# Kernel tuning notes

Hardware: AMD Instinct MI355X
Metric: run time of the kernel (lower is better)

The kernel has to match this reference:

```python
import jax, jax.numpy as jnp
import numpy as np

# ---- constants mirroring ATSSPostProcessor defaults / metainfo ----
PRE_NMS_THRESH = 0.05
PRE_NMS_TOP_N = 1000
NMS_THRESH = 0.6
POST_TOP_N = 100
IMG_H, IMG_W = 800.0, 1216.0      # metainfo img_shape
BW_XY, BW_WH = 10.0, 5.0          # GLIP/ATSS box coder weights (10,10,5,5)
MAX_DWH = float(np.log(1000.0 / 16.0))
CLASS_OFFSET = 10000.0            # batched_nms class offset (> max coord)


def setup_inputs() -> dict:
    key = jax.random.key(0)
    k0, k1, k2, k3 = jax.random.split(key, 4)
    N, C, L, H, W = 8, 80, 256, 100, 152
    box_regression = jax.random.normal(k0, (N, 4, H, W), jnp.float32)
    centerness = jax.random.normal(k1, (N, 1, H, W), jnp.float32)
    box_cls = jax.random.normal(k2, (N, C, H, W), jnp.float32)
    dot_product_logits = jax.random.normal(k3, (N, H * W, L), jnp.float32)
    # stride-8 grid anchors with base size 64
    ys, xs = np.meshgrid(np.arange(H), np.arange(W), indexing='ij')
    cx, cy = (xs + 0.5) * 8.0, (ys + 0.5) * 8.0
    anchors = jnp.asarray(
        np.stack([cx - 32, cy - 32, cx + 32, cy + 32], -1).reshape(-1, 4),
        jnp.float32)
    # MEAN aggregation positive map: class j <- tokens [3j, 3j+1, 3j+2]
    pm = np.zeros((C, L), np.float32)
    for j in range(C):
        pm[j, 3 * j:3 * j + 3] = 1.0 / 3.0
    pos_map = jnp.asarray(pm)
    return dict(box_regression=box_regression, centerness=centerness,
                box_cls=box_cls, dot_product_logits=dot_product_logits,
                anchors=anchors, pos_map=pos_map)


def _decode(a, r):
    # delta_xywh decode with weights (10,10,5,5), clamped to img_shape
    aw, ah = a[..., 2] - a[..., 0], a[..., 3] - a[..., 1]
    acx, acy = a[..., 0] + 0.5 * aw, a[..., 1] + 0.5 * ah
    dx, dy = r[..., 0] / BW_XY, r[..., 1] / BW_XY
    dw = jnp.minimum(r[..., 2] / BW_WH, MAX_DWH)
    dh = jnp.minimum(r[..., 3] / BW_WH, MAX_DWH)
    pcx, pcy = dx * aw + acx, dy * ah + acy
    pw, ph = jnp.exp(dw) * aw, jnp.exp(dh) * ah
    x1 = jnp.clip(pcx - 0.5 * pw, 0.0, IMG_W)
    y1 = jnp.clip(pcy - 0.5 * ph, 0.0, IMG_H)
    x2 = jnp.clip(pcx + 0.5 * pw, 0.0, IMG_W)
    y2 = jnp.clip(pcy + 0.5 * ph, 0.0, IMG_H)
    return jnp.stack([x1, y1, x2, y2], -1)


def _iou_matrix(b):  # b: [K,4]
    area = (b[:, 2] - b[:, 0]) * (b[:, 3] - b[:, 1])
    ix1 = jnp.maximum(b[:, None, 0], b[None, :, 0])
    iy1 = jnp.maximum(b[:, None, 1], b[None, :, 1])
    ix2 = jnp.minimum(b[:, None, 2], b[None, :, 2])
    iy2 = jnp.minimum(b[:, None, 3], b[None, :, 3])
    inter = jnp.maximum(ix2 - ix1, 0.0) * jnp.maximum(iy2 - iy1, 0.0)
    return inter / (area[:, None] + area[None, :] - inter + 1e-6)


def _nms_single(boxes, scores, labels, valid):
    # class-aware greedy NMS (batched_nms) on fixed-size K candidates
    K = boxes.shape[0]
    s = jnp.where(valid, scores, -1.0)
    order = jnp.argsort(-s)
    b, s, l, v = boxes[order], s[order], labels[order], valid[order]
    ob = b + (l.astype(b.dtype) * CLASS_OFFSET)[:, None]
    iou = _iou_matrix(ob)
    ar = jnp.arange(K)

    def body(i, keep):
        sup = keep[i] & (iou[i] > NMS_THRESH) & (ar > i)
        return keep & ~sup

    keep = jax.lax.fori_loop(0, K, body, v)
    s2 = jnp.where(keep, s, -1.0)
    topv, topi = jax.lax.top_k(s2, POST_TOP_N)
    good = topv > 0.0
    fb = jnp.where(good[:, None], b[topi], 0.0)
    fs = jnp.where(good, topv, 0.0)
    fl = jnp.where(good, l[topi], 0)
    return fb, fs, fl


def reference(box_regression, centerness, box_cls, dot_product_logits,
              anchors, pos_map):
    N = box_regression.shape[0]
    C = pos_map.shape[0]
    HW = anchors.shape[0]
    # permute_and_flatten: [N,4,H,W] -> [N,HW,4]
    reg = box_regression.transpose(0, 2, 3, 1).reshape(N, HW, 4)
    ctr = jax.nn.sigmoid(centerness.reshape(N, HW))
    # sigmoid score fusion + MEAN grounding->od aggregation
    dp = jax.nn.sigmoid(dot_product_logits)            # [N,HW,L]
    scores = jnp.einsum('nkl,cl->nkc', dp, pos_map)    # [N,HW,C]
    cand = scores > PRE_NMS_THRESH
    fused = scores * ctr[:, :, None]
    # dynamic per-image topk over candidates == fixed-K masked top_k
    masked = jnp.where(cand, fused, -1.0).reshape(N, HW * C)
    vals, idx = jax.lax.top_k(masked, PRE_NMS_TOP_N)   # [N,K]
    valid = jnp.take_along_axis(cand.reshape(N, -1), idx, axis=1)
    loc = idx // C
    labels = idx % C + 1
    a = anchors[loc]                                           # [N,K,4]
    r = jnp.take_along_axis(reg, loc[..., None], axis=1)       # [N,K,4]
    boxes = _decode(a, r)
    sc = jnp.sqrt(jnp.maximum(vals, 0.0))
    w = boxes[..., 2] - boxes[..., 0]
    h = boxes[..., 3] - boxes[..., 1]
    valid = valid & (w > 0) & (h > 0)  # min_size = 0 filter
    # scale_factor = 1.0 -> boxes unchanged
    out_boxes, out_scores, out_labels = jax.vmap(_nms_single)(
        boxes, sc, labels, valid)
    return out_boxes, out_scores, out_labels
```

## Files before the change

kernel.cpp:

```cpp
#include <hip/hip_runtime.h>
#include <hip/hip_bf16.h>

#define NIMG 8
#define NC   80
#define NL   256
#define HWQ  15200
#define TOPK 1000
#define CAP  4096
#define SSORT 2048
#define NPOST 100
#define PERIMG (HWQ * NC)
#define TOTAL (NIMG * PERIMG)
#define SROW 32
#define SBLK32 (NIMG * HWQ / SROW)
#define PI4  (PERIMG / 4)
#define WPI  (PI4 / 64)
#define NWAVE (NIMG * WPI)
#define CBLK (TOTAL / 4 / 256)

__device__ __forceinline__ unsigned flipKey(float f) {
    unsigned u = __float_as_uint(f);
    return u ^ (((unsigned)((int)u >> 31)) | 0x80000000u);
}
__device__ __forceinline__ float unflipKey(unsigned k) {
    unsigned u = k ^ ((k & 0x80000000u) ? 0x80000000u : 0xFFFFFFFFu);
    return __uint_as_float(u);
}
__device__ __forceinline__ float sigmoidf(float x) {
    return 1.0f / (1.0f + expf(-x));
}

__global__ void __launch_bounds__(256)
kinit(const float* __restrict__ pm, unsigned* nnz, unsigned* tok, float* wt,
      unsigned* __restrict__ gh) {
    int g = blockIdx.x * 256 + threadIdx.x;
    if (g < NIMG * 4096) gh[g] = 0;
    if (g < NC) {
        int c = g;
        int cnt = 0;
        for (int l = 0; l < NL; ++l) {
            float v = pm[c * NL + l];
            if (v != 0.0f) { tok[cnt * NC + c] = l; wt[cnt * NC + c] = v; cnt++; }
        }
        nnz[c] = cnt;
    }
}

__global__ void __launch_bounds__(512)
kscoreh(const float* __restrict__ dp, const float* __restrict__ cent,
        const unsigned* __restrict__ nnz, const unsigned* __restrict__ tok,
        const float* __restrict__ wt, float* __restrict__ scores,
        unsigned* __restrict__ gh) {
    __shared__ unsigned h[4096];
    __shared__ float sctr[SROW];
    int t = threadIdx.x;
    for (int i = t; i < 4096; i += 512) h[i] = 0;
    long long base = (long long)blockIdx.x * SROW;
    if (t < SROW) sctr[t] = sigmoidf(cent[base + t]);
    long long obase = base * NC;
    const float* dpb = dp + base * NL;

    int  rr[5], cc[5], mm[5];
    int  tk[5][3];
    float wv[5][3], xv[5][3];
#pragma unroll
    for (int j = 0; j < 5; ++j) {
        int o = t + j * 512;
        rr[j] = o / NC; cc[j] = o - rr[j] * NC;
        mm[j] = (int)nnz[cc[j]];
        int c = cc[j];
        tk[j][0] = (int)tok[c] & 255;
        tk[j][1] = (int)tok[NC + c] & 255;
        tk[j][2] = (int)tok[2 * NC + c] & 255;
        wv[j][0] = wt[c]; wv[j][1] = wt[NC + c]; wv[j][2] = wt[2 * NC + c];
    }
#pragma unroll
    for (int j = 0; j < 5; ++j) {
        const float* row = dpb + rr[j] * NL;
        if (tk[j][1] == tk[j][0] + 1 && tk[j][2] == tk[j][0] + 2) {
            float3 v3 = *(const float3*)(row + tk[j][0]);
            xv[j][0] = v3.x; xv[j][1] = v3.y; xv[j][2] = v3.z;
        } else {
            xv[j][0] = row[tk[j][0]];
            xv[j][1] = row[tk[j][1]];
            xv[j][2] = row[tk[j][2]];
        }
    }
    __syncthreads();
#pragma unroll
    for (int j = 0; j < 5; ++j) {
        float acc = 0.0f;
        if (mm[j] == 3) {
            float s0 = sigmoidf(xv[j][0]);
            float s1 = sigmoidf(xv[j][1]);
            float s2 = sigmoidf(xv[j][2]);
            acc += s0 * wv[j][0]; acc += s1 * wv[j][1]; acc += s2 * wv[j][2];
        } else {
            const float* row = dpb + rr[j] * NL;
            for (int q = 0; q < mm[j]; ++q)
                acc += sigmoidf(row[tok[q * NC + cc[j]]]) * wt[q * NC + cc[j]];
        }
        float sc = (acc > 0.05f) ? acc * sctr[rr[j]] : -1.0f;
        scores[obase + t + j * 512] = sc;
        atomicAdd(&h[flipKey(sc) >> 20], 1u);
    }
    __syncthreads();
    int n = (int)(base / HWQ);
    for (int i = t; i < 4096; i += 512)
        if (h[i]) atomicAdd(&gh[n * 4096 + i], h[i]);
}

__global__ void kfind1(const unsigned* __restrict__ gh, unsigned* meta) {
    __shared__ unsigned h[4096];
    __shared__ unsigned psum[256];
    int n = blockIdx.x;
    for (int i = threadIdx.x; i < 4096; i += 256) h[i] = gh[n * 4096 + i];
    __syncthreads();
    unsigned s = 0;
    for (int i = 0; i < 16; ++i) s += h[threadIdx.x * 16 + i];
    psum[threadIdx.x] = s;
    __syncthreads();
    if (threadIdx.x == 0) {
        unsigned cum = 0, above = 0; int B = 0; bool done = false;
        for (int seg = 255; seg >= 0 && !done; --seg) {
            if (cum + psum[seg] >= TOPK) {
                for (int b = seg * 16 + 15; b >= seg * 16; --b) {
                    if (cum + h[b] >= TOPK) { B = b; above = cum; done = true; break; }
                    cum += h[b];
                }
            } else cum += psum[seg];
        }
        meta[n] = (unsigned)B;
        meta[8 + n] = above;
    }
}

__global__ void __launch_bounds__(256)
kcountM(const float4* __restrict__ scores4, const unsigned* __restrict__ meta,
        unsigned* __restrict__ wavecnt, unsigned long long* __restrict__ wavemask) {
    int i4 = blockIdx.x * 256 + threadIdx.x;
    int n = i4 / PI4;
    unsigned B = meta[n];
    float4 v = scores4[i4];
    bool s0 = (flipKey(v.x) >> 20) >= B;
    bool s1 = (flipKey(v.y) >> 20) >= B;
    bool s2 = (flipKey(v.z) >> 20) >= B;
    bool s3 = (flipKey(v.w) >> 20) >= B;
    unsigned long long m0 = __ballot(s0);
    unsigned long long m1 = __ballot(s1);
    unsigned long long m2 = __ballot(s2);
    unsigned long long m3 = __ballot(s3);
    if ((threadIdx.x & 63) == 0) {
        int w = i4 >> 6;
        wavemask[(size_t)w * 4 + 0] = m0;
        wavemask[(size_t)w * 4 + 1] = m1;
        wavemask[(size_t)w * 4 + 2] = m2;
        wavemask[(size_t)w * 4 + 3] = m3;
        wavecnt[w] = (unsigned)(__popcll(m0) + __popcll(m1)
                              + __popcll(m2) + __popcll(m3));
    }
}

__global__ void __launch_bounds__(1024)
kscanW(const unsigned* __restrict__ wavecnt,
       const unsigned long long* __restrict__ wavemask,
       const float* __restrict__ scores,
       unsigned* __restrict__ cnt, unsigned long long* __restrict__ cand) {
    __shared__ unsigned ps[1024];
    int n = blockIdx.x, t = threadIdx.x;
    const unsigned* wc = wavecnt + n * WPI;
    int s0 = t * 5;
    unsigned loc[5], vv[5]; unsigned sum = 0;
#pragma unroll
    for (int j = 0; j < 5; ++j) {
        int i = s0 + j;
        unsigned x = (i < WPI) ? wc[i] : 0u;
        vv[j] = x; loc[j] = sum; sum += x;
    }
    ps[t] = sum;
    __syncthreads();
    for (int off = 1; off < 1024; off <<= 1) {
        unsigned add = (t >= off) ? ps[t - off] : 0u;
        __syncthreads();
        ps[t] += add;
        __syncthreads();
    }
    unsigned excl = (t > 0) ? ps[t - 1] : 0u;
    if (t == 1023) cnt[n] = ps[1023];
    const float* sb = scores + (size_t)n * PERIMG;
    unsigned long long* cb = cand + (size_t)n * CAP;
#pragma unroll
    for (int j = 0; j < 5; ++j) {
        int wl = s0 + j;
        if (wl < WPI && vv[j]) {
            unsigned off = excl + loc[j];
            const unsigned long long* mk = wavemask + ((size_t)(n * WPI + wl)) * 4;
#pragma unroll
            for (int e = 0; e < 4; ++e) {
                unsigned long long m = mk[e];
                while (m) {
                    int b = __ffsll(m) - 1; m &= m - 1;
                    int li = wl * 256 + b * 4 + e;
                    unsigned key = flipKey(sb[li]);
                    if (off < CAP)
                        cb[off] = ((unsigned long long)key << 32)
                                  | (unsigned)(~li);
                    off++;
                }
            }
        }
    }
}

__global__ void __launch_bounds__(256)
kcount(const float4* __restrict__ scores4, const unsigned* __restrict__ meta,
       unsigned* __restrict__ wavecnt) {
    int i4 = blockIdx.x * 256 + threadIdx.x;
    int n = i4 / PI4;
    unsigned B = meta[n];
    float4 v = scores4[i4];
    int ns = 0;
    ns += ((flipKey(v.x) >> 20) >= B);
    ns += ((flipKey(v.y) >> 20) >= B);
    ns += ((flipKey(v.z) >> 20) >= B);
    ns += ((flipKey(v.w) >> 20) >= B);
    int s = ns;
#pragma unroll
    for (int off = 1; off < 64; off <<= 1) s += __shfl_xor(s, off);
    if ((threadIdx.x & 63) == 0) wavecnt[i4 >> 6] = (unsigned)s;
}
__global__ void __launch_bounds__(1024)
kscan(const unsigned* __restrict__ wavecnt, unsigned* __restrict__ waveoff,
      unsigned* __restrict__ cnt) {
    __shared__ unsigned ps[1024];
    int n = blockIdx.x, t = threadIdx.x;
    const unsigned* wc = wavecnt + n * WPI;
    unsigned* wo = waveoff + n * WPI;
    int s0 = t * 5;
    unsigned loc[5]; unsigned sum = 0;
#pragma unroll
    for (int j = 0; j < 5; ++j) {
        int i = s0 + j;
        unsigned vv = (i < WPI) ? wc[i] : 0u;
        loc[j] = sum; sum += vv;
    }
    ps[t] = sum;
    __syncthreads();
    for (int off = 1; off < 1024; off <<= 1) {
        unsigned add = (t >= off) ? ps[t - off] : 0u;
        __syncthreads();
        ps[t] += add;
        __syncthreads();
    }
    unsigned excl = (t > 0) ? ps[t - 1] : 0u;
#pragma unroll
    for (int j = 0; j < 5; ++j) {
        int i = s0 + j;
        if (i < WPI) wo[i] = excl + loc[j];
    }
    if (t == 1023) cnt[n] = ps[1023];
}
__global__ void __launch_bounds__(256)
kwrite(const float4* __restrict__ scores4, const unsigned* __restrict__ meta,
       const unsigned* __restrict__ waveoff, unsigned long long* __restrict__ cand) {
    int i4 = blockIdx.x * 256 + threadIdx.x;
    int n = i4 / PI4;
    unsigned B = meta[n];
    float4 v = scores4[i4];
    int li0 = (i4 - n * PI4) * 4;
    unsigned keys[4]; int sel[4]; int ns = 0;
    keys[0] = flipKey(v.x); sel[0] = (keys[0] >> 20) >= B; ns += sel[0];
    keys[1] = flipKey(v.y); sel[1] = (keys[1] >> 20) >= B; ns += sel[1];
    keys[2] = flipKey(v.z); sel[2] = (keys[2] >> 20) >= B; ns += sel[2];
    keys[3] = flipKey(v.w); sel[3] = (keys[3] >> 20) >= B; ns += sel[3];
    int lane = threadIdx.x & 63;
    int pre = ns;
#pragma unroll
    for (int off = 1; off < 64; off <<= 1) {
        int o = __shfl_up(pre, off);
        if (lane >= off) pre += o;
    }
    unsigned base = waveoff[i4 >> 6] + (unsigned)(pre - ns);
    unsigned long long* cbase = cand + (size_t)n * CAP;
#pragma unroll
    for (int e = 0; e < 4; ++e) {
        if (sel[e]) {
            if (base < CAP)
                cbase[base] = ((unsigned long long)keys[e] << 32)
                              | (unsigned)(~(li0 + e));
            base++;
        }
    }
}

__global__ void __launch_bounds__(1024)
kfine(const unsigned long long* __restrict__ cand, const unsigned* __restrict__ cnt,
      const unsigned* __restrict__ meta, unsigned long long* __restrict__ sorted) {
    __shared__ unsigned h[4096];
    __shared__ unsigned long long sbuf[SSORT];
    __shared__ unsigned psum[256];
    __shared__ unsigned selcnt;
    __shared__ unsigned Fbin;
    int n = blockIdx.x, t = threadIdx.x;
    int M = min(cnt[n], (unsigned)CAP);
    unsigned B = meta[n], above = meta[8 + n];
    const unsigned long long* cb = cand + (size_t)n * CAP;
    for (int i = t; i < 4096; i += 1024) h[i] = 0;
    sbuf[t] = 0ULL; sbuf[t + 1024] = 0ULL;
    if (t == 0) selcnt = 0;
    __syncthreads();
    for (int i = t; i < M; i += 1024) {
        unsigned key = (unsigned)(cb[i] >> 32);
        if ((key >> 20) == B) atomicAdd(&h[(key >> 8) & 0xFFFu], 1u);
    }
    __syncthreads();
    if (t < 256) {
        unsigned s = 0;
        for (int i = 0; i < 16; ++i) s += h[t * 16 + i];
        psum[t] = s;
    }
    __syncthreads();
    if (t == 0) {
        unsigned cum = above; int F = 0; bool done = false;
        for (int seg = 255; seg >= 0 && !done; --seg) {
            if (cum + psum[seg] >= TOPK) {
                for (int b = seg * 16 + 15; b >= seg * 16; --b) {
                    if (cum + h[b] >= TOPK) { F = b; done = true; break; }
                    cum += h[b];
                }
            } else cum += psum[seg];
        }
        Fbin = (unsigned)F;
    }
    __syncthreads();
    unsigned T24 = (B << 12) | Fbin;
    for (int i = t; i < M; i += 1024) {
        unsigned long long e = cb[i];
        unsigned key = (unsigned)(e >> 32);
        if ((key >> 8) >= T24) {
            unsigned p = atomicAdd(&selcnt, 1u);
            if (p < SSORT) sbuf[p] = e;
        }
    }
    __syncthreads();
    int s = (int)selcnt;
    int SN = (s <= 1024) ? 1024 : SSORT;
    for (int k = 2; k <= SN; k <<= 1) {
        for (int j = k >> 1; j > 0; j >>= 1) {
            for (int i = t; i < SN; i += 1024) {
                int l = i ^ j;
                if (l > i) {
                    unsigned long long a = sbuf[i], b = sbuf[l];
                    bool sw = ((i & k) == 0) ? (a < b) : (a > b);
                    if (sw) { sbuf[i] = b; sbuf[l] = a; }
                }
            }
            __syncthreads();
        }
    }
    if (t < TOPK) sorted[(n << 10) + t] = sbuf[t];
}

__global__ void __launch_bounds__(256)
kdecode(const unsigned long long* __restrict__ sorted,
        const float* __restrict__ anchors, const float* __restrict__ breg,
        float4* __restrict__ box4, float4* __restrict__ obx4,
        float* __restrict__ areag, unsigned* __restrict__ lblkeep) {
    int gid = blockIdx.x * 256 + threadIdx.x;
    if (gid >= NIMG * TOPK) return;
    int n = gid / TOPK, r = gid - n * TOPK;
    int o = (n << 10) + r;
    unsigned long long e = sorted[o];
    unsigned key = (unsigned)(e >> 32);
    bool real = key > 0x80000000u;
    unsigned li = ~(unsigned)(e & 0xFFFFFFFFu);
    unsigned k = li / NC, c = li - k * NC;
    int label = (int)c + 1;
    float x1 = 0, y1 = 0, x2 = 0, y2 = 0;
    bool val = false;
    if (real) {
        float a0 = anchors[k * 4 + 0], a1 = anchors[k * 4 + 1];
        float a2 = anchors[k * 4 + 2], a3 = anchors[k * 4 + 3];
        float r0 = breg[(n * 4 + 0) * HWQ + k];
        float r1 = breg[(n * 4 + 1) * HWQ + k];
        float r2 = breg[(n * 4 + 2) * HWQ + k];
        float r3 = breg[(n * 4 + 3) * HWQ + k];
        float aw = a2 - a0, ah = a3 - a1;
        float acx = a0 + 0.5f * aw, acy = a1 + 0.5f * ah;
        float dx = r0 / 10.0f, dy = r1 / 10.0f;
        float dw = fminf(r2 / 5.0f, 4.135166556742356f);
        float dh = fminf(r3 / 5.0f, 4.135166556742356f);
        float pcx = dx * aw + acx, pcy = dy * ah + acy;
        float pw = expf(dw) * aw, ph = expf(dh) * ah;
        x1 = fminf(fmaxf(pcx - 0.5f * pw, 0.0f), 1216.0f);
        y1 = fminf(fmaxf(pcy - 0.5f * ph, 0.0f), 800.0f);
        x2 = fminf(fmaxf(pcx + 0.5f * pw, 0.0f), 1216.0f);
        y2 = fminf(fmaxf(pcy + 0.5f * ph, 0.0f), 800.0f);
        val = (x2 - x1 > 0.0f) && (y2 - y1 > 0.0f);
    }
    box4[o] = make_float4(x1, y1, x2, y2);
    float off = (float)label * 10000.0f;
    float o0 = x1 + off, o1 = y1 + off, o2 = x2 + off, o3 = y2 + off;
    obx4[o] = make_float4(o0, o1, o2, o3);
    areag[o] = (o2 - o0) * (o3 - o1);
    lblkeep[o] = (unsigned)(real ? label : 0) | ((val ? 1u : 0u) << 16);
}

__global__ void __launch_bounds__(1024)
knms2(const unsigned long long* __restrict__ sorted,
      const float4* __restrict__ obx4, const float* __restrict__ areag,
      const unsigned* __restrict__ lblkeep, const float4* __restrict__ box4,
      float* __restrict__ outBoxes, float* __restrict__ outScores,
      float* __restrict__ outLabels) {
    __shared__ float ob0[TOPK], ob1[TOPK], ob2[TOPK], ob3[TOPK], area[TOPK];
    __shared__ unsigned long long sup[TOPK];
    __shared__ unsigned short lbl[TOPK];
    __shared__ unsigned char  keepf[TOPK];
    __shared__ unsigned short wrank[TOPK];
    __shared__ unsigned short clist[TOPK];
    __shared__ unsigned short cstart[NC + 1];
    __shared__ unsigned ccnt[NC];
    __shared__ int pfx[1024];
    __shared__ int smax;

    int n = blockIdx.x, t = threadIdx.x;
    if (t < NC) ccnt[t] = 0;
    if (t == 0) smax = 0;
    if (t < TOPK) {
        int o = (n << 10) + t;
        float4 ob = obx4[o];
        ob0[t] = ob.x; ob1[t] = ob.y; ob2[t] = ob.z; ob3[t] = ob.w;
        area[t] = areag[o];
        unsigned lk = lblkeep[o];
        lbl[t] = (unsigned short)(lk & 0xFFFFu);
        keepf[t] = (unsigned char)(lk >> 16);
        sup[t] = 0ULL;
    }
    __syncthreads();

    if (t < TOPK) {
        unsigned short my = lbl[t];
        int w = 0;
        if (my) {
            for (int r = 0; r < t; ++r) w += (lbl[r] == my);
            atomicAdd(&ccnt[my - 1], 1u);
        }
        wrank[t] = (unsigned short)w;
    }
    __syncthreads();
    if (t < NC) atomicMax(&smax, (int)ccnt[t]);
    __syncthreads();
    if (t == 0) {
        unsigned s = 0;
        for (int c = 0; c < NC; ++c) { cstart[c] = (unsigned short)s; s += ccnt[c]; }
        cstart[NC] = (unsigned short)s;
    }
    __syncthreads();
    if (t < TOPK && lbl[t]) clist[cstart[lbl[t] - 1] + wrank[t]] = (unsigned short)t;
    __syncthreads();

    if (smax <= 64) {
        if (t < TOPK && lbl[t]) {
            int base = cstart[lbl[t] - 1];
            int w = wrank[t];
            float A0 = ob0[t], A1 = ob1[t], A2 = ob2[t], A3 = ob3[t], Aa = area[t];
            unsigned long long m = 0ULL;
            for (int j = 0; j < w; ++j) {
                int ib = clist[base + j];
                float iw = fminf(A2, ob2[ib]) - fmaxf(A0, ob0[ib]);
                float ih = fminf(A3, ob3[ib]) - fmaxf(A1, ob1[ib]);
                float inter = fmaxf(iw, 0.0f) * fmaxf(ih, 0.0f);
                float denom = Aa + area[ib] - inter + 1e-6f;
                if (inter / denom > 0.6f) m |= (1ull << j);
            }
            sup[t] = m;
        }
        __syncthreads();
        if (t < NC) {
            unsigned long long kb = 0ULL;
            int base = cstart[t], mc = (int)ccnt[t];
            for (int w = 0; w < mc; ++w) {
                int i = clist[base + w];
                bool kp = keepf[i] && ((sup[i] & kb) == 0ULL);
                keepf[i] = kp ? 1 : 0;
                if (kp) kb |= (1ull << w);
            }
        }
    } else {
        __syncthreads();
        if (t < NC) {
            int s0 = cstart[t], s1 = s0 + (int)ccnt[t];
            for (int a = s0; a < s1; ++a) {
                int ia = clist[a];
                if (!keepf[ia]) continue;
                float A0 = ob0[ia], A1 = ob1[ia], A2 = ob2[ia], A3 = ob3[ia];
                float Aa = area[ia];
                for (int b = a + 1; b < s1; ++b) {
                    int ib = clist[b];
                    if (!keepf[ib]) continue;
                    float iw = fminf(A2, ob2[ib]) - fmaxf(A0, ob0[ib]);
                    float ih = fminf(A3, ob3[ib]) - fmaxf(A1, ob1[ib]);
                    float inter = fmaxf(iw, 0.0f) * fmaxf(ih, 0.0f);
                    float denom = Aa + area[ib] - inter + 1e-6f;
                    if (inter / denom > 0.6f) keepf[ib] = 0;
                }
            }
        }
    }
    __syncthreads();

    pfx[t] = (t < TOPK) ? (int)keepf[t] : 0;
    __syncthreads();
    for (int off = 1; off < 1024; off <<= 1) {
        int add = (t >= off) ? pfx[t - off] : 0;
        __syncthreads();
        pfx[t] += add;
        __syncthreads();
    }
    int total = pfx[1023];

    if (t < TOPK && keepf[t]) {
        int q = pfx[t] - 1;
        if (q < NPOST) {
            int o = (n << 10) + t;
            float4 b = box4[o];
            float fused = unflipKey((unsigned)(sorted[o] >> 32));
            outBoxes[(n * NPOST + q) * 4 + 0] = b.x;
            outBoxes[(n * NPOST + q) * 4 + 1] = b.y;
            outBoxes[(n * NPOST + q) * 4 + 2] = b.z;
            outBoxes[(n * NPOST + q) * 4 + 3] = b.w;
            outScores[n * NPOST + q] = sqrtf(fmaxf(fused, 0.0f));
            outLabels[n * NPOST + q] = (float)lbl[t];
        }
    }
    if (t < NPOST && t >= total) {
        outBoxes[(n * NPOST + t) * 4 + 0] = 0.0f;
        outBoxes[(n * NPOST + t) * 4 + 1] = 0.0f;
        outBoxes[(n * NPOST + t) * 4 + 2] = 0.0f;
        outBoxes[(n * NPOST + t) * 4 + 3] = 0.0f;
        outScores[n * NPOST + t] = 0.0f;
        outLabels[n * NPOST + t] = 0.0f;
    }
}

extern "C" void kernel_launch(void* const* d_in, const int* in_sizes, int n_in,
                              void* d_out, int out_size, void* d_ws, size_t ws_size,
                              hipStream_t stream) {
    const float* breg = (const float*)d_in[0];
    const float* cent = (const float*)d_in[1];
    const float* dp   = (const float*)d_in[3];
    const float* anc  = (const float*)d_in[4];
    const float* pm   = (const float*)d_in[5];

    char* ws = (char*)d_ws;
    size_t off_scores  = 0;
    size_t off_gh      = off_scores + (size_t)TOTAL * 4;
    size_t off_cnt     = off_gh + (size_t)NIMG * 4096 * 4;
    size_t off_meta    = off_cnt + 128;
    size_t off_cand    = off_meta + 128;
    size_t off_nnz     = off_cand + (size_t)NIMG * CAP * 8;
    size_t off_tok     = off_nnz + 512;
    size_t off_wt      = off_tok + (size_t)NC * NL * 4;
    size_t off_wavecnt = off_wt + (size_t)NC * NL * 4;
    size_t off_tail    = off_wavecnt + (size_t)NWAVE * 4 + 64;
    size_t needed_new  = off_tail + (size_t)NWAVE * 32;
    size_t needed_old  = off_tail + (size_t)NWAVE * 4 + 64;
    if (ws_size < needed_old) return;
    bool useMask = ws_size >= needed_new;

    size_t off_sorted = off_scores;
    size_t off_box4   = off_sorted + (size_t)NIMG * 1024 * 8;
    size_t off_obx4   = off_box4 + (size_t)NIMG * 1024 * 16;
    size_t off_area   = off_obx4 + (size_t)NIMG * 1024 * 16;
    size_t off_lblk   = off_area + (size_t)NIMG * 1024 * 4;

    float*    scores  = (float*)(ws + off_scores);
    unsigned* gh      = (unsigned*)(ws + off_gh);
    unsigned* cnt     = (unsigned*)(ws + off_cnt);
    unsigned* meta    = (unsigned*)(ws + off_meta);
    unsigned long long* cand = (unsigned long long*)(ws + off_cand);
    unsigned* nnz     = (unsigned*)(ws + off_nnz);
    unsigned* tok     = (unsigned*)(ws + off_tok);
    float*    wt      = (float*)(ws + off_wt);
    unsigned* wavecnt = (unsigned*)(ws + off_wavecnt);
    unsigned long long* wavemask = (unsigned long long*)(ws + off_tail);
    unsigned* waveoff = (unsigned*)(ws + off_tail);
    unsigned long long* sorted = (unsigned long long*)(ws + off_sorted);
    float4*   box4    = (float4*)(ws + off_box4);
    float4*   obx4    = (float4*)(ws + off_obx4);
    float*    areag   = (float*)(ws + off_area);
    unsigned* lblkeep = (unsigned*)(ws + off_lblk);

    kinit<<<128, 256, 0, stream>>>(pm, nnz, tok, wt, gh);
    kscoreh<<<SBLK32, 512, 0, stream>>>(dp, cent, nnz, tok, wt, scores, gh);
    kfind1<<<NIMG, 256, 0, stream>>>(gh, meta);
    if (useMask) {
        kcountM<<<CBLK, 256, 0, stream>>>((const float4*)scores, meta,
                                          wavecnt, wavemask);
        kscanW<<<NIMG, 1024, 0, stream>>>(wavecnt, wavemask, scores, cnt, cand);
    } else {
        kcount<<<CBLK, 256, 0, stream>>>((const float4*)scores, meta, wavecnt);
        kscan<<<NIMG, 1024, 0, stream>>>(wavecnt, waveoff, cnt);
        kwrite<<<CBLK, 256, 0, stream>>>((const float4*)scores, meta, waveoff, cand);
    }
    kfine<<<NIMG, 1024, 0, stream>>>(cand, cnt, meta, sorted);
    kdecode<<<(NIMG * TOPK + 255) / 256, 256, 0, stream>>>(sorted, anc, breg,
                                                           box4, obx4, areag, lblkeep);

    float* outBoxes  = (float*)d_out;
    float* outScores = outBoxes + NIMG * NPOST * 4;
    float* outLabels = outScores + NIMG * NPOST;
    knms2<<<NIMG, 1024, 0, stream>>>(sorted, obx4, areag, lblkeep, box4,
                                     outBoxes, outScores, outLabels);
}
```

Baseline: 198.0 us.

## Stage sigmoid of full logit rows in LDS with coalesced float4 loads per wave

```diff
diff --git a/kernel.cpp b/kernel.cpp
--- a/kernel.cpp
+++ b/kernel.cpp
@@ -11,8 +11,8 @@
 #define NPOST 100
 #define PERIMG (HWQ * NC)
 #define TOTAL (NIMG * PERIMG)
-#define SROW 32
-#define SBLK32 (NIMG * HWQ / SROW)
+#define RPB  16
+#define SBLKR (NIMG * HWQ / RPB)
 #define PI4  (PERIMG / 4)
 #define WPI  (PI4 / 64)
 #define NWAVE (NIMG * WPI)
@@ -52,60 +52,55 @@
         const float* __restrict__ wt, float* __restrict__ scores,
         unsigned* __restrict__ gh) {
     __shared__ unsigned h[4096];
-    __shared__ float sctr[SROW];
+    __shared__ float sig[8][2][NL];
     int t = threadIdx.x;
+    int wid = t >> 6, lane = t & 63;
     for (int i = t; i < 4096; i += 512) h[i] = 0;
-    long long base = (long long)blockIdx.x * SROW;
-    if (t < SROW) sctr[t] = sigmoidf(cent[base + t]);
-    long long obase = base * NC;
-    const float* dpb = dp + base * NL;
-
-    int  rr[5], cc[5], mm[5];
-    int  tk[5][3];
-    float wv[5][3], xv[5][3];
-#pragma unroll
-    for (int j = 0; j < 5; ++j) {
-        int o = t + j * 512;
-        rr[j] = o / NC; cc[j] = o - rr[j] * NC;
-        mm[j] = (int)nnz[cc[j]];
-        int c = cc[j];
-        tk[j][0] = (int)tok[c] & 255;
-        tk[j][1] = (int)tok[NC + c] & 255;
-        tk[j][2] = (int)tok[2 * NC + c] & 255;
-        wv[j][0] = wt[c]; wv[j][1] = wt[NC + c]; wv[j][2] = wt[2 * NC + c];
-    }
-#pragma unroll
-    for (int j = 0; j < 5; ++j) {
-        const float* row = dpb + rr[j] * NL;
-        if (tk[j][1] == tk[j][0] + 1 && tk[j][2] == tk[j][0] + 2) {
-            float3 v3 = *(const float3*)(row + tk[j][0]);
-            xv[j][0] = v3.x; xv[j][1] = v3.y; xv[j][2] = v3.z;
-        } else {
-            xv[j][0] = row[tk[j][0]];
-            xv[j][1] = row[tk[j][1]];
-            xv[j][2] = row[tk[j][2]];
-        }
-    }
-    __syncthreads();
-#pragma unroll
-    for (int j = 0; j < 5; ++j) {
-        float acc = 0.0f;
-        if (mm[j] == 3) {
-            float s0 = sigmoidf(xv[j][0]);
-            float s1 = sigmoidf(xv[j][1]);
-            float s2 = sigmoidf(xv[j][2]);
-            acc += s0 * wv[j][0]; acc += s1 * wv[j][1]; acc += s2 * wv[j][2];
-        } else {
-            const float* row = dpb + rr[j] * NL;
-            for (int q = 0; q < mm[j]; ++q)
-                acc += sigmoidf(row[tok[q * NC + cc[j]]]) * wt[q * NC + cc[j]];
-        }
-        float sc = (acc > 0.05f) ? acc * sctr[rr[j]] : -1.0f;
-        scores[obase + t + j * 512] = sc;
-        atomicAdd(&h[flipKey(sc) >> 20], 1u);
-    }
-    __syncthreads();
-    int n = (int)(base / HWQ);
+    __syncthreads();
+    long long brow = (long long)blockIdx.x * RPB;
+    const float4* dp4 = (const float4*)dp;
+    float ctr2[2];
+#pragma unroll
+    for (int rr = 0; rr < 2; ++rr) {
+        long long row = brow + wid * 2 + rr;
+        float4 v = dp4[row * (NL / 4) + lane];
+        sig[wid][rr][lane * 4 + 0] = sigmoidf(v.x);
+        sig[wid][rr][lane * 4 + 1] = sigmoidf(v.y);
+        sig[wid][rr][lane * 4 + 2] = sigmoidf(v.z);
+        sig[wid][rr][lane * 4 + 3] = sigmoidf(v.w);
+        ctr2[rr] = sigmoidf(cent[row]);
+    }
+#pragma unroll
+    for (int p = 0; p < 2; ++p) {
+        int c = lane + p * 64;
+        if (c < NC) {
+            int m = (int)nnz[c];
+            int t0 = (int)tok[c] & 255;
+            int t1 = (int)tok[NC + c] & 255;
+            int t2 = (int)tok[2 * NC + c] & 255;
+            float w0 = wt[c], w1 = wt[NC + c], w2 = wt[2 * NC + c];
+#pragma unroll
+            for (int rr = 0; rr < 2; ++rr) {
+                long long row = brow + wid * 2 + rr;
+                const float* sg = sig[wid][rr];
+                float acc = 0.0f;
+                if (m == 3) {
+                    float s0 = sg[t0];
+                    float s1 = sg[t1];
+                    float s2 = sg[t2];
+                    acc += s0 * w0; acc += s1 * w1; acc += s2 * w2;
+                } else {
+                    for (int q = 0; q < m; ++q)
+                        acc += sg[(int)tok[q * NC + c] & 255] * wt[q * NC + c];
+                }
+                float sc = (acc > 0.05f) ? acc * ctr2[rr] : -1.0f;
+                scores[row * NC + c] = sc;
+                atomicAdd(&h[flipKey(sc) >> 20], 1u);
+            }
+        }
+    }
+    __syncthreads();
+    int n = (int)(brow / HWQ);
     for (int i = t; i < 4096; i += 512)
         if (h[i]) atomicAdd(&gh[n * 4096 + i], h[i]);
 }
@@ -592,7 +587,7 @@
     unsigned* lblkeep = (unsigned*)(ws + off_lblk);
 
     kinit<<<128, 256, 0, stream>>>(pm, nnz, tok, wt, gh);
-    kscoreh<<<SBLK32, 512, 0, stream>>>(dp, cent, nnz, tok, wt, scores, gh);
+    kscoreh<<<SBLKR, 512, 0, stream>>>(dp, cent, nnz, tok, wt, scores, gh);
     kfind1<<<NIMG, 256, 0, stream>>>(gh, meta);
     if (useMask) {
         kcountM<<<CBLK, 256, 0, stream>>>((const float4*)scores, meta,
```

New measurement: 212.7 us. 1.07x slower.

## Fuse candidate scan, fine select, sort, decode and NMS into one per-image kernel

Applied to the files above, without the earlier changes.

```diff
diff --git a/kernel.cpp b/kernel.cpp
--- a/kernel.cpp
+++ b/kernel.cpp
@@ -6,7 +6,6 @@
 #define NL   256
 #define HWQ  15200
 #define TOPK 1000
-#define CAP  4096
 #define SSORT 2048
 #define NPOST 100
 #define PERIMG (HWQ * NC)
@@ -162,158 +161,55 @@
 }
 
 __global__ void __launch_bounds__(1024)
-kscanW(const unsigned* __restrict__ wavecnt,
-       const unsigned long long* __restrict__ wavemask,
-       const float* __restrict__ scores,
-       unsigned* __restrict__ cnt, unsigned long long* __restrict__ cand) {
-    __shared__ unsigned ps[1024];
+ktail(const unsigned* __restrict__ wavecnt,
+      const unsigned long long* __restrict__ wavemask,
+      const float* __restrict__ scores, const unsigned* __restrict__ meta,
+      const float* __restrict__ anchors, const float* __restrict__ breg,
+      float* __restrict__ outBoxes, float* __restrict__ outScores,
+      float* __restrict__ outLabels) {
+    __shared__ unsigned long long sbuf[SSORT];
+    __shared__ unsigned uover[4096];
+    __shared__ float area[TOPK];
+    __shared__ unsigned long long sup[TOPK];
+    __shared__ unsigned short lbl[TOPK];
+    __shared__ unsigned char  keepf[TOPK];
+    __shared__ unsigned short wrank[TOPK];
+    __shared__ unsigned short clist[TOPK];
+    __shared__ unsigned short cstart[NC + 1];
+    __shared__ unsigned ccnt[NC];
+    __shared__ int pfx[1024];
+    __shared__ unsigned selcnt, FbinS;
+    __shared__ int smax;
+
     int n = blockIdx.x, t = threadIdx.x;
+    unsigned B = meta[n], above = meta[8 + n];
     const unsigned* wc = wavecnt + n * WPI;
-    int s0 = t * 5;
-    unsigned loc[5], vv[5]; unsigned sum = 0;
-#pragma unroll
-    for (int j = 0; j < 5; ++j) {
-        int i = s0 + j;
-        unsigned x = (i < WPI) ? wc[i] : 0u;
-        vv[j] = x; loc[j] = sum; sum += x;
-    }
-    ps[t] = sum;
-    __syncthreads();
-    for (int off = 1; off < 1024; off <<= 1) {
-        unsigned add = (t >= off) ? ps[t - off] : 0u;
-        __syncthreads();
-        ps[t] += add;
-        __syncthreads();
-    }
-    unsigned excl = (t > 0) ? ps[t - 1] : 0u;
-    if (t == 1023) cnt[n] = ps[1023];
+    const unsigned long long* wm = wavemask + (size_t)n * WPI * 4;
     const float* sb = scores + (size_t)n * PERIMG;
-    unsigned long long* cb = cand + (size_t)n * CAP;
-#pragma unroll
-    for (int j = 0; j < 5; ++j) {
-        int wl = s0 + j;
-        if (wl < WPI && vv[j]) {
-            unsigned off = excl + loc[j];
-            const unsigned long long* mk = wavemask + ((size_t)(n * WPI + wl)) * 4;
+
+    unsigned* h = uover;
+    for (int i = t; i < 4096; i += 1024) h[i] = 0;
+    sbuf[t] = 0ULL; sbuf[t + 1024] = 0ULL;
+    if (t == 0) { selcnt = 0; smax = 0; }
+    if (t < NC) ccnt[t] = 0;
+    __syncthreads();
+
+    for (int wl = t; wl < WPI; wl += 1024) {
+        if (wc[wl]) {
 #pragma unroll
             for (int e = 0; e < 4; ++e) {
-                unsigned long long m = mk[e];
+                unsigned long long m = wm[(size_t)wl * 4 + e];
                 while (m) {
                     int b = __ffsll(m) - 1; m &= m - 1;
-                    int li = wl * 256 + b * 4 + e;
-                    unsigned key = flipKey(sb[li]);
-                    if (off < CAP)
-                        cb[off] = ((unsigned long long)key << 32)
-                                  | (unsigned)(~li);
-                    off++;
-                }
-            }
-        }
-    }
-}
-
-__global__ void __launch_bounds__(256)
-kcount(const float4* __restrict__ scores4, const unsigned* __restrict__ meta,
-       unsigned* __restrict__ wavecnt) {
-    int i4 = blockIdx.x * 256 + threadIdx.x;
-    int n = i4 / PI4;
-    unsigned B = meta[n];
-    float4 v = scores4[i4];
-    int ns = 0;
-    ns += ((flipKey(v.x) >> 20) >= B);
-    ns += ((flipKey(v.y) >> 20) >= B);
-    ns += ((flipKey(v.z) >> 20) >= B);
-    ns += ((flipKey(v.w) >> 20) >= B);
-    int s = ns;
-#pragma unroll
-    for (int off = 1; off < 64; off <<= 1) s += __shfl_xor(s, off);
-    if ((threadIdx.x & 63) == 0) wavecnt[i4 >> 6] = (unsigned)s;
-}
-__global__ void __launch_bounds__(1024)
-kscan(const unsigned* __restrict__ wavecnt, unsigned* __restrict__ waveoff,
-      unsigned* __restrict__ cnt) {
-    __shared__ unsigned ps[1024];
-    int n = blockIdx.x, t = threadIdx.x;
-    const unsigned* wc = wavecnt + n * WPI;
-    unsigned* wo = waveoff + n * WPI;
-    int s0 = t * 5;
-    unsigned loc[5]; unsigned sum = 0;
-#pragma unroll
-    for (int j = 0; j < 5; ++j) {
-        int i = s0 + j;
-        unsigned vv = (i < WPI) ? wc[i] : 0u;
-        loc[j] = sum; sum += vv;
-    }
-    ps[t] = sum;
-    __syncthreads();
-    for (int off = 1; off < 1024; off <<= 1) {
-        unsigned add = (t >= off) ? ps[t - off] : 0u;
-        __syncthreads();
-        ps[t] += add;
-        __syncthreads();
-    }
-    unsigned excl = (t > 0) ? ps[t - 1] : 0u;
-#pragma unroll
-    for (int j = 0; j < 5; ++j) {
-        int i = s0 + j;
-        if (i < WPI) wo[i] = excl + loc[j];
-    }
-    if (t == 1023) cnt[n] = ps[1023];
-}
-__global__ void __launch_bounds__(256)
-kwrite(const float4* __restrict__ scores4, const unsigned* __restrict__ meta,
-       const unsigned* __restrict__ waveoff, unsigned long long* __restrict__ cand) {
-    int i4 = blockIdx.x * 256 + threadIdx.x;
-    int n = i4 / PI4;
-    unsigned B = meta[n];
-    float4 v = scores4[i4];
-    int li0 = (i4 - n * PI4) * 4;
-    unsigned keys[4]; int sel[4]; int ns = 0;
-    keys[0] = flipKey(v.x); sel[0] = (keys[0] >> 20) >= B; ns += sel[0];
-    keys[1] = flipKey(v.y); sel[1] = (keys[1] >> 20) >= B; ns += sel[1];
-    keys[2] = flipKey(v.z); sel[2] = (keys[2] >> 20) >= B; ns += sel[2];
-    keys[3] = flipKey(v.w); sel[3] = (keys[3] >> 20) >= B; ns += sel[3];
-    int lane = threadIdx.x & 63;
-    int pre = ns;
-#pragma unroll
-    for (int off = 1; off < 64; off <<= 1) {
-        int o = __shfl_up(pre, off);
-        if (lane >= off) pre += o;
-    }
-    unsigned base = waveoff[i4 >> 6] + (unsigned)(pre - ns);
-    unsigned long long* cbase = cand + (size_t)n * CAP;
-#pragma unroll
-    for (int e = 0; e < 4; ++e) {
-        if (sel[e]) {
-            if (base < CAP)
-                cbase[base] = ((unsigned long long)keys[e] << 32)
-                              | (unsigned)(~(li0 + e));
-            base++;
-        }
-    }
-}
-
-__global__ void __launch_bounds__(1024)
-kfine(const unsigned long long* __restrict__ cand, const unsigned* __restrict__ cnt,
-      const unsigned* __restrict__ meta, unsigned long long* __restrict__ sorted) {
-    __shared__ unsigned h[4096];
-    __shared__ unsigned long long sbuf[SSORT];
-    __shared__ unsigned psum[256];
-    __shared__ unsigned selcnt;
-    __shared__ unsigned Fbin;
-    int n = blockIdx.x, t = threadIdx.x;
-    int M = min(cnt[n], (unsigned)CAP);
-    unsigned B = meta[n], above = meta[8 + n];
-    const unsigned long long* cb = cand + (size_t)n * CAP;
-    for (int i = t; i < 4096; i += 1024) h[i] = 0;
-    sbuf[t] = 0ULL; sbuf[t + 1024] = 0ULL;
-    if (t == 0) selcnt = 0;
-    __syncthreads();
-    for (int i = t; i < M; i += 1024) {
-        unsigned key = (unsigned)(cb[i] >> 32);
-        if ((key >> 20) == B) atomicAdd(&h[(key >> 8) & 0xFFFu], 1u);
-    }
-    __syncthreads();
+                    unsigned key = flipKey(sb[wl * 256 + b * 4 + e]);
+                    if ((key >> 20) == B) atomicAdd(&h[(key >> 8) & 0xFFFu], 1u);
+                }
+            }
+        }
+    }
+    __syncthreads();
+
+    unsigned* psum = (unsigned*)pfx;
     if (t < 256) {
         unsigned s = 0;
         for (int i = 0; i < 16; ++i) s += h[t * 16 + i];
@@ -330,21 +226,33 @@
                 }
             } else cum += psum[seg];
         }
-        Fbin = (unsigned)F;
-    }
-    __syncthreads();
-    unsigned T24 = (B << 12) | Fbin;
-    for (int i = t; i < M; i += 1024) {
-        unsigned long long e = cb[i];
-        unsigned key = (unsigned)(e >> 32);
-        if ((key >> 8) >= T24) {
-            unsigned p = atomicAdd(&selcnt, 1u);
-            if (p < SSORT) sbuf[p] = e;
-        }
-    }
-    __syncthreads();
-    int s = (int)selcnt;
-    int SN = (s <= 1024) ? 1024 : SSORT;
+        FbinS = (unsigned)F;
+    }
+    __syncthreads();
+    unsigned T24 = (B << 12) | FbinS;
+
+    for (int wl = t; wl < WPI; wl += 1024) {
+        if (wc[wl]) {
+#pragma unroll
+            for (int e = 0; e < 4; ++e) {
+                unsigned long long m = wm[(size_t)wl * 4 + e];
+                while (m) {
+                    int b = __ffsll(m) - 1; m &= m - 1;
+                    int li = wl * 256 + b * 4 + e;
+                    unsigned key = flipKey(sb[li]);
+                    if ((key >> 8) >= T24) {
+                        unsigned p = atomicAdd(&selcnt, 1u);
+                        if (p < SSORT)
+                            sbuf[p] = ((unsigned long long)key << 32)
+                                      | (unsigned)(~li);
+                    }
+                }
+            }
+        }
+    }
+    __syncthreads();
+
+    int SN = ((int)selcnt <= 1024) ? 1024 : SSORT;
     for (int k = 2; k <= SN; k <<= 1) {
         for (int j = k >> 1; j > 0; j >>= 1) {
             for (int i = t; i < SN; i += 1024) {
@@ -358,82 +266,46 @@
             __syncthreads();
         }
     }
-    if (t < TOPK) sorted[(n << 10) + t] = sbuf[t];
-}
-
-__global__ void __launch_bounds__(256)
-kdecode(const unsigned long long* __restrict__ sorted,
-        const float* __restrict__ anchors, const float* __restrict__ breg,
-        float4* __restrict__ box4, float4* __restrict__ obx4,
-        float* __restrict__ areag, unsigned* __restrict__ lblkeep) {
-    int gid = blockIdx.x * 256 + threadIdx.x;
-    if (gid >= NIMG * TOPK) return;
-    int n = gid / TOPK, r = gid - n * TOPK;
-    int o = (n << 10) + r;
-    unsigned long long e = sorted[o];
-    unsigned key = (unsigned)(e >> 32);
-    bool real = key > 0x80000000u;
-    unsigned li = ~(unsigned)(e & 0xFFFFFFFFu);
-    unsigned k = li / NC, c = li - k * NC;
-    int label = (int)c + 1;
-    float x1 = 0, y1 = 0, x2 = 0, y2 = 0;
-    bool val = false;
-    if (real) {
-        float a0 = anchors[k * 4 + 0], a1 = anchors[k * 4 + 1];
-        float a2 = anchors[k * 4 + 2], a3 = anchors[k * 4 + 3];
-        float r0 = breg[(n * 4 + 0) * HWQ + k];
-        float r1 = breg[(n * 4 + 1) * HWQ + k];
-        float r2 = breg[(n * 4 + 2) * HWQ + k];
-        float r3 = breg[(n * 4 + 3) * HWQ + k];
-        float aw = a2 - a0, ah = a3 - a1;
-        float acx = a0 + 0.5f * aw, acy = a1 + 0.5f * ah;
-        float dx = r0 / 10.0f, dy = r1 / 10.0f;
-        float dw = fminf(r2 / 5.0f, 4.135166556742356f);
-        float dh = fminf(r3 / 5.0f, 4.135166556742356f);
-        float pcx = dx * aw + acx, pcy = dy * ah + acy;
-        float pw = expf(dw) * aw, ph = expf(dh) * ah;
-        x1 = fminf(fmaxf(pcx - 0.5f * pw, 0.0f), 1216.0f);
-        y1 = fminf(fmaxf(pcy - 0.5f * ph, 0.0f), 800.0f);
-        x2 = fminf(fmaxf(pcx + 0.5f * pw, 0.0f), 1216.0f);
-        y2 = fminf(fmaxf(pcy + 0.5f * ph, 0.0f), 800.0f);
-        val = (x2 - x1 > 0.0f) && (y2 - y1 > 0.0f);
-    }
-    box4[o] = make_float4(x1, y1, x2, y2);
-    float off = (float)label * 10000.0f;
-    float o0 = x1 + off, o1 = y1 + off, o2 = x2 + off, o3 = y2 + off;
-    obx4[o] = make_float4(o0, o1, o2, o3);
-    areag[o] = (o2 - o0) * (o3 - o1);
-    lblkeep[o] = (unsigned)(real ? label : 0) | ((val ? 1u : 0u) << 16);
-}
-
-__global__ void __launch_bounds__(1024)
-knms2(const unsigned long long* __restrict__ sorted,
-      const float4* __restrict__ obx4, const float* __restrict__ areag,
-      const unsigned* __restrict__ lblkeep, const float4* __restrict__ box4,
-      float* __restrict__ outBoxes, float* __restrict__ outScores,
-      float* __restrict__ outLabels) {
-    __shared__ float ob0[TOPK], ob1[TOPK], ob2[TOPK], ob3[TOPK], area[TOPK];
-    __shared__ unsigned long long sup[TOPK];
-    __shared__ unsigned short lbl[TOPK];
-    __shared__ unsigned char  keepf[TOPK];
-    __shared__ unsigned short wrank[TOPK];
-    __shared__ unsigned short clist[TOPK];
-    __shared__ unsigned short cstart[NC + 1];
-    __shared__ unsigned ccnt[NC];
-    __shared__ int pfx[1024];
-    __shared__ int smax;
-
-    int n = blockIdx.x, t = threadIdx.x;
-    if (t < NC) ccnt[t] = 0;
-    if (t == 0) smax = 0;
+
+    float* ob0 = (float*)uover;
+    float* ob1 = ob0 + TOPK;
+    float* ob2 = ob1 + TOPK;
+    float* ob3 = ob2 + TOPK;
     if (t < TOPK) {
-        int o = (n << 10) + t;
-        float4 ob = obx4[o];
-        ob0[t] = ob.x; ob1[t] = ob.y; ob2[t] = ob.z; ob3[t] = ob.w;
-        area[t] = areag[o];
-        unsigned lk = lblkeep[o];
-        lbl[t] = (unsigned short)(lk & 0xFFFFu);
-        keepf[t] = (unsigned char)(lk >> 16);
+        unsigned long long e = sbuf[t];
+        unsigned key = (unsigned)(e >> 32);
+        bool real = key > 0x80000000u;
+        unsigned li = ~(unsigned)(e & 0xFFFFFFFFu);
+        unsigned k = li / NC, c = li - k * NC;
+        int label = (int)c + 1;
+        float x1 = 0, y1 = 0, x2 = 0, y2 = 0;
+        bool val = false;
+        if (real) {
+            float a0 = anchors[k * 4 + 0], a1 = anchors[k * 4 + 1];
+            float a2 = anchors[k * 4 + 2], a3 = anchors[k * 4 + 3];
+            float r0 = breg[(n * 4 + 0) * HWQ + k];
+            float r1 = breg[(n * 4 + 1) * HWQ + k];
+            float r2 = breg[(n * 4 + 2) * HWQ + k];
+            float r3 = breg[(n * 4 + 3) * HWQ + k];
+            float aw = a2 - a0, ah = a3 - a1;
+            float acx = a0 + 0.5f * aw, acy = a1 + 0.5f * ah;
+            float dx = r0 / 10.0f, dy = r1 / 10.0f;
+            float dw = fminf(r2 / 5.0f, 4.135166556742356f);
+            float dh = fminf(r3 / 5.0f, 4.135166556742356f);
+            float pcx = dx * aw + acx, pcy = dy * ah + acy;
+            float pw = expf(dw) * aw, ph = expf(dh) * ah;
+            x1 = fminf(fmaxf(pcx - 0.5f * pw, 0.0f), 1216.0f);
+            y1 = fminf(fmaxf(pcy - 0.5f * ph, 0.0f), 800.0f);
+            x2 = fminf(fmaxf(pcx + 0.5f * pw, 0.0f), 1216.0f);
+            y2 = fminf(fmaxf(pcy + 0.5f * ph, 0.0f), 800.0f);
+            val = (x2 - x1 > 0.0f) && (y2 - y1 > 0.0f);
+        }
+        float off = (float)label * 10000.0f;
+        ob0[t] = x1 + off; ob1[t] = y1 + off;
+        ob2[t] = x2 + off; ob3[t] = y2 + off;
+        area[t] = (ob2[t] - ob0[t]) * (ob3[t] - ob1[t]);
+        lbl[t] = real ? (unsigned short)label : (unsigned short)0;
+        keepf[t] = val ? 1 : 0;
         sup[t] = 0ULL;
     }
     __syncthreads();
@@ -522,13 +394,31 @@
     if (t < TOPK && keepf[t]) {
         int q = pfx[t] - 1;
         if (q < NPOST) {
-            int o = (n << 10) + t;
-            float4 b = box4[o];
-            float fused = unflipKey((unsigned)(sorted[o] >> 32));
-            outBoxes[(n * NPOST + q) * 4 + 0] = b.x;
-            outBoxes[(n * NPOST + q) * 4 + 1] = b.y;
-            outBoxes[(n * NPOST + q) * 4 + 2] = b.z;
-            outBoxes[(n * NPOST + q) * 4 + 3] = b.w;
+            unsigned long long e = sbuf[t];
+            unsigned li = ~(unsigned)(e & 0xFFFFFFFFu);
+            unsigned k = li / NC;
+            float a0 = anchors[k * 4 + 0], a1 = anchors[k * 4 + 1];
+            float a2 = anchors[k * 4 + 2], a3 = anchors[k * 4 + 3];
+            float r0 = breg[(n * 4 + 0) * HWQ + k];
+            float r1 = breg[(n * 4 + 1) * HWQ + k];
+            float r2 = breg[(n * 4 + 2) * HWQ + k];
+            float r3 = breg[(n * 4 + 3) * HWQ + k];
+            float aw = a2 - a0, ah = a3 - a1;
+            float acx = a0 + 0.5f * aw, acy = a1 + 0.5f * ah;
+            float dx = r0 / 10.0f, dy = r1 / 10.0f;
+            float dw = fminf(r2 / 5.0f, 4.135166556742356f);
+            float dh = fminf(r3 / 5.0f, 4.135166556742356f);
+            float pcx = dx * aw + acx, pcy = dy * ah + acy;
+            float pw = expf(dw) * aw, ph = expf(dh) * ah;
+            float x1 = fminf(fmaxf(pcx - 0.5f * pw, 0.0f), 1216.0f);
+            float y1 = fminf(fmaxf(pcy - 0.5f * ph, 0.0f), 800.0f);
+            float x2 = fminf(fmaxf(pcx + 0.5f * pw, 0.0f), 1216.0f);
+            float y2 = fminf(fmaxf(pcy + 0.5f * ph, 0.0f), 800.0f);
+            float fused = unflipKey((unsigned)(e >> 32));
+            outBoxes[(n * NPOST + q) * 4 + 0] = x1;
+            outBoxes[(n * NPOST + q) * 4 + 1] = y1;
+            outBoxes[(n * NPOST + q) * 4 + 2] = x2;
+            outBoxes[(n * NPOST + q) * 4 + 3] = y2;
             outScores[n * NPOST + q] = sqrtf(fmaxf(fused, 0.0f));
             outLabels[n * NPOST + q] = (float)lbl[t];
         }
@@ -553,63 +443,35 @@
     const float* pm   = (const float*)d_in[5];
 
     char* ws = (char*)d_ws;
-    size_t off_scores  = 0;
-    size_t off_gh      = off_scores + (size_t)TOTAL * 4;
-    size_t off_cnt     = off_gh + (size_t)NIMG * 4096 * 4;
-    size_t off_meta    = off_cnt + 128;
-    size_t off_cand    = off_meta + 128;
-    size_t off_nnz     = off_cand + (size_t)NIMG * CAP * 8;
-    size_t off_tok     = off_nnz + 512;
-    size_t off_wt      = off_tok + (size_t)NC * NL * 4;
-    size_t off_wavecnt = off_wt + (size_t)NC * NL * 4;
-    size_t off_tail    = off_wavecnt + (size_t)NWAVE * 4 + 64;
-    size_t needed_new  = off_tail + (size_t)NWAVE * 32;
-    size_t needed_old  = off_tail + (size_t)NWAVE * 4 + 64;
-    if (ws_size < needed_old) return;
-    bool useMask = ws_size >= needed_new;
-
-    size_t off_sorted = off_scores;
-    size_t off_box4   = off_sorted + (size_t)NIMG * 1024 * 8;
-    size_t off_obx4   = off_box4 + (size_t)NIMG * 1024 * 16;
-    size_t off_area   = off_obx4 + (size_t)NIMG * 1024 * 16;
-    size_t off_lblk   = off_area + (size_t)NIMG * 1024 * 4;
+    size_t off_scores   = 0;
+    size_t off_gh       = off_scores + (size_t)TOTAL * 4;
+    size_t off_meta     = off_gh + (size_t)NIMG * 4096 * 4;
+    size_t off_nnz      = off_meta + 128;
+    size_t off_tok      = off_nnz + 512;
+    size_t off_wt       = off_tok + (size_t)NC * NL * 4;
+    size_t off_wavecnt  = off_wt + (size_t)NC * NL * 4;
+    size_t off_wavemask = off_wavecnt + (size_t)NWAVE * 4 + 64;
+    size_t needed       = off_wavemask + (size_t)NWAVE * 32;
+    if (ws_size < needed) return;
 
     float*    scores  = (float*)(ws + off_scores);
     unsigned* gh      = (unsigned*)(ws + off_gh);
-    unsigned* cnt     = (unsigned*)(ws + off_cnt);
     unsigned* meta    = (unsigned*)(ws + off_meta);
-    unsigned long long* cand = (unsigned long long*)(ws + off_cand);
     unsigned* nnz     = (unsigned*)(ws + off_nnz);
     unsigned* tok     = (unsigned*)(ws + off_tok);
     float*    wt      = (float*)(ws + off_wt);
     unsigned* wavecnt = (unsigned*)(ws + off_wavecnt);
-    unsigned long long* wavemask = (unsigned long long*)(ws + off_tail);
-    unsigned* waveoff = (unsigned*)(ws + off_tail);
-    unsigned long long* sorted = (unsigned long long*)(ws + off_sorted);
-    float4*   box4    = (float4*)(ws + off_box4);
-    float4*   obx4    = (float4*)(ws + off_obx4);
-    float*    areag   = (float*)(ws + off_area);
-    unsigned* lblkeep = (unsigned*)(ws + off_lblk);
+    unsigned long long* wavemask = (unsigned long long*)(ws + off_wavemask);
 
     kinit<<<128, 256, 0, stream>>>(pm, nnz, tok, wt, gh);
     kscoreh<<<SBLK32, 512, 0, stream>>>(dp, cent, nnz, tok, wt, scores, gh);
     kfind1<<<NIMG, 256, 0, stream>>>(gh, meta);
-    if (useMask) {
-        kcountM<<<CBLK, 256, 0, stream>>>((const float4*)scores, meta,
-                                          wavecnt, wavemask);
-        kscanW<<<NIMG, 1024, 0, stream>>>(wavecnt, wavemask, scores, cnt, cand);
-    } else {
-        kcount<<<CBLK, 256, 0, stream>>>((const float4*)scores, meta, wavecnt);
-        kscan<<<NIMG, 1024, 0, stream>>>(wavecnt, waveoff, cnt);
-        kwrite<<<CBLK, 256, 0, stream>>>((const float4*)scores, meta, waveoff, cand);
-    }
-    kfine<<<NIMG, 1024, 0, stream>>>(cand, cnt, meta, sorted);
-    kdecode<<<(NIMG * TOPK + 255) / 256, 256, 0, stream>>>(sorted, anc, breg,
-                                                           box4, obx4, areag, lblkeep);
+    kcountM<<<CBLK, 256, 0, stream>>>((const float4*)scores, meta,
+                                      wavecnt, wavemask);
 
     float* outBoxes  = (float*)d_out;
     float* outScores = outBoxes + NIMG * NPOST * 4;
     float* outLabels = outScores + NIMG * NPOST;
-    knms2<<<NIMG, 1024, 0, stream>>>(sorted, obx4, areag, lblkeep, box4,
-                                     outBoxes, outScores, outLabels);
-}
+    ktail<<<NIMG, 1024, 0, stream>>>(wavecnt, wavemask, scores, meta,
+                                     anc, breg, outBoxes, outScores, outLabels);
+}
```

Result: slower. 211.8 us (+7.0%).
